# Kernel optimization log

Measured on AMD Instinct MI355X. Metric: run time of the kernel, lower is better.

## Reference

```python
import jax, jax.numpy as jnp
import numpy as np

B, S, D, H, DFF = 2, 2048, 2048, 16, 8192
DH = D // H
EPS = 1e-5


def _layer_norm(x, g, b):
    mu = jnp.mean(x, axis=-1, keepdims=True)
    var = jnp.mean(jnp.square(x - mu), axis=-1, keepdims=True)
    return (x - mu) * jax.lax.rsqrt(var + EPS) * g + b


def setup_inputs() -> dict:
    key = jax.random.key(0)
    ks = jax.random.split(key, 12)
    sc = 0.02
    inp = {
        "x": jax.random.normal(ks[0], (B, S, D), dtype=jnp.float32),
        # attention projections, stored [in, out] (torch Linear weight transposed)
        "wq": jax.random.normal(ks[1], (D, D), dtype=jnp.float32) * sc,
        "bq": jnp.zeros((D,), jnp.float32),
        "wk": jax.random.normal(ks[2], (D, D), dtype=jnp.float32) * sc,
        "bk": jnp.zeros((D,), jnp.float32),
        "wv": jax.random.normal(ks[3], (D, D), dtype=jnp.float32) * sc,
        "bv": jnp.zeros((D,), jnp.float32),
        "wo": jax.random.normal(ks[4], (D, D), dtype=jnp.float32) * sc,
        "bo": jnp.zeros((D,), jnp.float32),
        "ln1_g": jnp.ones((D,), jnp.float32),
        "ln1_b": jnp.zeros((D,), jnp.float32),
        # feed-forward
        "w1": jax.random.normal(ks[5], (D, DFF), dtype=jnp.float32) * sc,
        "b1": jnp.zeros((DFF,), jnp.float32),
        "w2": jax.random.normal(ks[6], (DFF, D), dtype=jnp.float32) * sc,
        "b2": jnp.zeros((D,), jnp.float32),
        "ln2_g": jnp.ones((D,), jnp.float32),
        "ln2_b": jnp.zeros((D,), jnp.float32),
    }
    return inp


def reference(x, wq, bq, wk, bk, wv, bv, wo, bo, ln1_g, ln1_b,
              w1, b1, w2, b2, ln2_g, ln2_b):
    # ---- MultiHeadAttentionBlock: x + MHA(LN(x)) ----
    h = _layer_norm(x, ln1_g, ln1_b)                      # [B,S,D]
    q = (h @ wq + bq).reshape(B, S, H, DH).transpose(0, 2, 1, 3)  # [B,H,S,DH]
    k = (h @ wk + bk).reshape(B, S, H, DH).transpose(0, 2, 1, 3)
    v = (h @ wv + bv).reshape(B, S, H, DH).transpose(0, 2, 1, 3)

    # faithful to source: scale by sqrt(d_dim), NOT sqrt(head_dim)
    scores = jnp.einsum("bhqd,bhkd->bhqk", q, k) / np.sqrt(D).astype(np.float32)
    # faithful triu/transpose masking (softmax sees raw zeros, not -inf)
    t = jnp.triu(scores).swapaxes(-2, -1)                 # [B,H,S,S]
    s = jax.nn.softmax(t, axis=-2)
    r = jnp.triu(s).swapaxes(-2, -1)
    attn = jnp.einsum("bhqk,bhkd->bhqd", r, v)            # [B,H,S,DH]
    attn = attn.transpose(0, 2, 1, 3).reshape(B, S, D)
    x = x + attn @ wo + bo

    # ---- FeedForwardBlock: x + FF(LN(x)), dropout rate 0 ----
    h2 = _layer_norm(x, ln2_g, ln2_b)
    ff = jax.nn.relu(h2 @ w1 + b1) @ w2 + b2
    return x + ff
```

## Files before the change

kernel.cpp:

```cpp
#include <hip/hip_runtime.h>


typedef unsigned short ushort_t;
typedef unsigned int   uint32;
typedef __attribute__((ext_vector_type(8))) short    short8;
typedef __attribute__((ext_vector_type(8))) ushort_t ushort8;
typedef __attribute__((ext_vector_type(4))) float    f32x4;

#define BDIM   2
#define SEQ    2048
#define DMODEL 2048
#define NHEAD  16
#define DHEAD  128
#define DFFN   8192
#define MROWS  (BDIM*SEQ)

#define GPTR(p) (const __attribute__((address_space(1))) void*)((const void*)(p))
#define SPTR(p) (__attribute__((address_space(3))) void*)((void*)(p))

__device__ __forceinline__ float bf2f(ushort_t u) {
  union { uint32 i; float f; } c; c.i = ((uint32)u) << 16; return c.f;
}
__device__ __forceinline__ ushort_t f2bf(float f) {
  union { float f; uint32 i; } c; c.f = f;
  uint32 u = c.i;
  return (ushort_t)((u + 0x7fffu + ((u >> 16) & 1u)) >> 16);
}

__global__ __launch_bounds__(256) void transpose_f32_bf16_kern(
    const float* __restrict__ W, ushort_t* __restrict__ Wt, int K, int N)
{
  __shared__ float tile[32][33];
  const int nb = blockIdx.x * 32, kb = blockIdx.y * 32;
  const int tx = threadIdx.x & 31, ty = threadIdx.x >> 5;
#pragma unroll
  for (int j = 0; j < 32; j += 8)
    tile[ty + j][tx] = W[(size_t)(kb + ty + j) * N + nb + tx];
  __syncthreads();
#pragma unroll
  for (int j = 0; j < 32; j += 8)
    Wt[(size_t)(nb + ty + j) * K + kb + tx] = f2bf(tile[tx][ty + j]);
}

__global__ __launch_bounds__(256) void ln_kern(
    const float* __restrict__ X, const float* __restrict__ G,
    const float* __restrict__ Bb, ushort_t* __restrict__ Out)
{
  const int row = blockIdx.x, tid = threadIdx.x;
  const float* xr = X + (size_t)row * DMODEL;
  float4 v0 = ((const float4*)xr)[tid * 2];
  float4 v1 = ((const float4*)xr)[tid * 2 + 1];
  float s  = v0.x + v0.y + v0.z + v0.w + v1.x + v1.y + v1.z + v1.w;
  float ss = v0.x*v0.x + v0.y*v0.y + v0.z*v0.z + v0.w*v0.w
           + v1.x*v1.x + v1.y*v1.y + v1.z*v1.z + v1.w*v1.w;
#pragma unroll
  for (int off = 32; off > 0; off >>= 1) {
    s  += __shfl_down(s, off);
    ss += __shfl_down(ss, off);
  }
  __shared__ float rs[4], rss[4];
  __shared__ float sh_mu, sh_rst;
  const int wv = tid >> 6;
  if ((tid & 63) == 0) { rs[wv] = s; rss[wv] = ss; }
  __syncthreads();
  if (tid == 0) {
    float S1 = rs[0] + rs[1] + rs[2] + rs[3];
    float S2 = rss[0] + rss[1] + rss[2] + rss[3];
    float mu = S1 * (1.f / DMODEL);
    float var = S2 * (1.f / DMODEL) - mu * mu;
    sh_mu = mu;
    sh_rst = rsqrtf(var + 1e-5f);
  }
  __syncthreads();
  const float mu = sh_mu, rst = sh_rst;
  float4 g0 = ((const float4*)G)[tid * 2];
  float4 g1 = ((const float4*)G)[tid * 2 + 1];
  float4 b0 = ((const float4*)Bb)[tid * 2];
  float4 b1 = ((const float4*)Bb)[tid * 2 + 1];
  ushort8 o;
  o[0] = f2bf((v0.x - mu) * rst * g0.x + b0.x);
  o[1] = f2bf((v0.y - mu) * rst * g0.y + b0.y);
  o[2] = f2bf((v0.z - mu) * rst * g0.z + b0.z);
  o[3] = f2bf((v0.w - mu) * rst * g0.w + b0.w);
  o[4] = f2bf((v1.x - mu) * rst * g1.x + b1.x);
  o[5] = f2bf((v1.y - mu) * rst * g1.y + b1.y);
  o[6] = f2bf((v1.z - mu) * rst * g1.z + b1.z);
  o[7] = f2bf((v1.w - mu) * rst * g1.w + b1.w);
  *(ushort8*)(Out + (size_t)row * DMODEL + tid * 8) = o;
}

template<int OUT_BF16, int RELU, int RESID>
__global__ __launch_bounds__(512, 2) void gemm_pipe_kern(
    const ushort_t* __restrict__ A, const ushort_t* __restrict__ Bt,
    const float* __restrict__ bias, const float* __restrict__ resid,
    void* __restrict__ Cout, int M, int N, int K)
{
  __shared__ ushort_t sA[3 * 128 * 32];
  __shared__ ushort_t sB[3 * 256 * 32];

  const int tid = threadIdx.x;
  const int nbx = gridDim.x;
  const int nwg = nbx * gridDim.y;
  const int bid = blockIdx.y * nbx + blockIdx.x;
  const int cpx = nwg >> 3;
  const int swz = (bid & 7) * cpx + (bid >> 3);
  const int n0 = (swz % nbx) * 256;
  const int m0 = (swz / nbx) * 128;

  const int l  = tid & 63, w = tid >> 6;
  const int lr = l & 15, lg = l >> 4;
  const int wr = w >> 2, wc = w & 3;

  const int srow = tid >> 2;
  const int schunk = ((tid & 3) ^ ((tid >> 3) & 3)) * 8;
  const ushort_t* Asrc  = A  + (size_t)(m0 + srow) * K + schunk;
  const ushort_t* Bsrc0 = Bt + (size_t)(n0 + srow) * K + schunk;
  const ushort_t* Bsrc1 = Bt + (size_t)(n0 + 128 + srow) * K + schunk;
  ushort_t* sAd = sA + tid * 8;
  ushort_t* sBd = sB + tid * 8;

  const int rdoff = ((lg ^ ((lr >> 1) & 3))) * 8;
  const int arow = (wr * 64 + lr) * 32 + rdoff;
  const int brow = (wc * 64 + lr) * 32 + rdoff;

  f32x4 acc[4][4] = {};
  const int T = K >> 5;

#define STAGE_AB0(d, kt) do { \
    __builtin_amdgcn_global_load_lds(GPTR(Asrc  + (size_t)(kt) * 32), SPTR(sAd + (d) * 4096), 16, 0, 0); \
    __builtin_amdgcn_global_load_lds(GPTR(Bsrc0 + (size_t)(kt) * 32), SPTR(sBd + (d) * 8192), 16, 0, 0); \
  } while (0)
#define STAGE_B1(d, kt) \
    __builtin_amdgcn_global_load_lds(GPTR(Bsrc1 + (size_t)(kt) * 32), SPTR(sBd + (d) * 8192 + 4096), 16, 0, 0)

  STAGE_AB0(0, 0); STAGE_B1(0, 0);
  STAGE_AB0(1, 1); STAGE_B1(1, 1);
  asm volatile("s_waitcnt vmcnt(3)" ::: "memory");
  __builtin_amdgcn_s_barrier();
  __builtin_amdgcn_sched_barrier(0);

  int cur = 0;
  for (int t = 0; t < T; ++t) {
    const int nxt2 = (cur == 0) ? 2 : cur - 1;
    const ushort_t* pA = sA + cur * 4096;
    const ushort_t* pB = sB + cur * 8192;

    short8 af0 = *(const short8*)(pA + arow);
    short8 af1 = *(const short8*)(pA + arow + 512);
    short8 af2 = *(const short8*)(pA + arow + 1024);
    short8 af3 = *(const short8*)(pA + arow + 1536);
    short8 bf0 = *(const short8*)(pB + brow);
    short8 bf1 = *(const short8*)(pB + brow + 512);
    if (t + 2 < T) STAGE_AB0(nxt2, t + 2);
    __builtin_amdgcn_s_barrier();
    asm volatile("s_waitcnt lgkmcnt(0)" ::: "memory");
    __builtin_amdgcn_sched_barrier(0);
    __builtin_amdgcn_s_setprio(1);
    acc[0][0] = __builtin_amdgcn_mfma_f32_16x16x32_bf16(af0, bf0, acc[0][0], 0, 0, 0);
    acc[1][0] = __builtin_amdgcn_mfma_f32_16x16x32_bf16(af1, bf0, acc[1][0], 0, 0, 0);
    acc[2][0] = __builtin_amdgcn_mfma_f32_16x16x32_bf16(af2, bf0, acc[2][0], 0, 0, 0);
    acc[3][0] = __builtin_amdgcn_mfma_f32_16x16x32_bf16(af3, bf0, acc[3][0], 0, 0, 0);
    acc[0][1] = __builtin_amdgcn_mfma_f32_16x16x32_bf16(af0, bf1, acc[0][1], 0, 0, 0);
    acc[1][1] = __builtin_amdgcn_mfma_f32_16x16x32_bf16(af1, bf1, acc[1][1], 0, 0, 0);
    acc[2][1] = __builtin_amdgcn_mfma_f32_16x16x32_bf16(af2, bf1, acc[2][1], 0, 0, 0);
    acc[3][1] = __builtin_amdgcn_mfma_f32_16x16x32_bf16(af3, bf1, acc[3][1], 0, 0, 0);
    __builtin_amdgcn_s_setprio(0);
    __builtin_amdgcn_s_barrier();

    short8 bf2 = *(const short8*)(pB + brow + 1024);
    short8 bf3 = *(const short8*)(pB + brow + 1536);
    if (t + 2 < T) STAGE_B1(nxt2, t + 2);
    __builtin_amdgcn_s_barrier();
    asm volatile("s_waitcnt lgkmcnt(0)" ::: "memory");
    __builtin_amdgcn_sched_barrier(0);
    __builtin_amdgcn_s_setprio(1);
    acc[0][2] = __builtin_amdgcn_mfma_f32_16x16x32_bf16(af0, bf2, acc[0][2], 0, 0, 0);
    acc[1][2] = __builtin_amdgcn_mfma_f32_16x16x32_bf16(af1, bf2, acc[1][2], 0, 0, 0);
    acc[2][2] = __builtin_amdgcn_mfma_f32_16x16x32_bf16(af2, bf2, acc[2][2], 0, 0, 0);
    acc[3][2] = __builtin_amdgcn_mfma_f32_16x16x32_bf16(af3, bf2, acc[3][2], 0, 0, 0);
    acc[0][3] = __builtin_amdgcn_mfma_f32_16x16x32_bf16(af0, bf3, acc[0][3], 0, 0, 0);
    acc[1][3] = __builtin_amdgcn_mfma_f32_16x16x32_bf16(af1, bf3, acc[1][3], 0, 0, 0);
    acc[2][3] = __builtin_amdgcn_mfma_f32_16x16x32_bf16(af2, bf3, acc[2][3], 0, 0, 0);
    acc[3][3] = __builtin_amdgcn_mfma_f32_16x16x32_bf16(af3, bf3, acc[3][3], 0, 0, 0);
    __builtin_amdgcn_s_setprio(0);
    if (t + 2 < T) { asm volatile("s_waitcnt vmcnt(3)" ::: "memory"); }
    else           { asm volatile("s_waitcnt vmcnt(0)" ::: "memory"); }
    __builtin_amdgcn_s_barrier();
    __builtin_amdgcn_sched_barrier(0);
    cur = (cur == 2) ? 0 : cur + 1;
  }
#undef STAGE_AB0
#undef STAGE_B1

#pragma unroll
  for (int mi = 0; mi < 4; ++mi) {
#pragma unroll
    for (int ni = 0; ni < 4; ++ni) {
      const int gn = n0 + wc * 64 + ni * 16 + lr;
      const float bvv = bias[gn];
#pragma unroll
      for (int j = 0; j < 4; ++j) {
        const int gm = m0 + wr * 64 + mi * 16 + lg * 4 + j;
        float v = acc[mi][ni][j] + bvv;
        if (RESID) v += resid[(size_t)gm * N + gn];
        if (RELU) v = fmaxf(v, 0.f);
        if (OUT_BF16) ((ushort_t*)Cout)[(size_t)gm * N + gn] = f2bf(v);
        else          ((float*)Cout)[(size_t)gm * N + gn] = v;
      }
    }
  }
}

__global__ __launch_bounds__(256) void attn_stats_kern(
    const ushort_t* __restrict__ Q, const ushort_t* __restrict__ Kb,
    float* __restrict__ E, float* __restrict__ DG)
{
  __shared__ ushort_t Ksm[64 * 128];
  const int qb = blockIdx.x;
  const int bh = blockIdx.y;
  const int b = bh >> 4, h = bh & 15;
  const int tid = threadIdx.x;
  const int l = tid & 63, w = tid >> 6;
  const int lr = l & 15, lg = l >> 4;

  const int qrow0 = qb * 64 + w * 16;

  const size_t qoff = (size_t)(b * SEQ + qrow0 + lr) * DMODEL + h * DHEAD + lg * 8;
  short8 af[4];
#pragma unroll
  for (int c = 0; c < 4; ++c) af[c] = *(const short8*)(Q + qoff + c * 32);

  const int srow_b = w * 16 + (l >> 4);
  const ushort_t* Kg = Kb + (size_t)b * SEQ * DMODEL + (size_t)h * DHEAD;
  ushort_t* Sbase = Ksm + w * 2048;

  f32x4 sume = {0.f, 0.f, 0.f, 0.f};
  f32x4 dge  = {0.f, 0.f, 0.f, 0.f};
  const float scale = 0.0220970869120796f;
  const int rx = lr & 7;

  for (int kc = qb; kc < 32; ++kc) {
    __syncthreads();
#pragma unroll
    for (int c = 0; c < 4; ++c) {
      const int row = srow_b + c * 4;
      const int g = (l & 15) ^ (row & 7);
      __builtin_amdgcn_global_load_lds(
          GPTR(Kg + (size_t)(kc * 64 + row) * DMODEL + g * 8),
          SPTR(Sbase + c * 512), 16, 0, 0);
    }
    __syncthreads();

    const int ks0 = (kc == qb) ? w : 0;
    for (int ks = ks0; ks < 4; ++ks) {
      short8 bfr[4];
#pragma unroll
      for (int c = 0; c < 4; ++c)
        bfr[c] = *(const short8*)(Ksm + (ks * 16 + lr) * 128 + ((lg + c * 4) ^ rx) * 8);
      f32x4 sc = {0.f, 0.f, 0.f, 0.f};
      sc = __builtin_amdgcn_mfma_f32_16x16x32_bf16(af[0], bfr[0], sc, 0, 0, 0);
      sc = __builtin_amdgcn_mfma_f32_16x16x32_bf16(af[1], bfr[1], sc, 0, 0, 0);
      sc = __builtin_amdgcn_mfma_f32_16x16x32_bf16(af[2], bfr[2], sc, 0, 0, 0);
      sc = __builtin_amdgcn_mfma_f32_16x16x32_bf16(af[3], bfr[3], sc, 0, 0, 0);
      if (kc == qb && ks == w) {
        const int ki = kc * 64 + ks * 16 + lr;
#pragma unroll
        for (int j = 0; j < 4; ++j) {
          const int qi = qrow0 + lg * 4 + j;
          if (ki >= qi) {
            float e = __expf(sc[j] * scale);
            sume[j] += e;
            if (ki == qi) dge[j] += e;
          }
        }
      } else {
#pragma unroll
        for (int j = 0; j < 4; ++j)
          sume[j] += __expf(sc[j] * scale);
      }
    }
  }

#pragma unroll
  for (int j = 0; j < 4; ++j) {
#pragma unroll
    for (int off = 1; off < 16; off <<= 1) {
      sume[j] += __shfl_xor(sume[j], off);
      dge[j]  += __shfl_xor(dge[j], off);
    }
  }
  if (lr == 0) {
#pragma unroll
    for (int j = 0; j < 4; ++j) {
      E[(size_t)bh * SEQ + qrow0 + lg * 4 + j]  = sume[j];
      DG[(size_t)bh * SEQ + qrow0 + lg * 4 + j] = dge[j];
    }
  }
}

__global__ __launch_bounds__(128) void vchunk_kern(
    const ushort_t* __restrict__ V, float* __restrict__ CS)
{
  const int c = blockIdx.x, bh = blockIdx.y;
  const int b = bh >> 4, h = bh & 15;
  const int dh = threadIdx.x;
  const ushort_t* vp = V + (size_t)(b * SEQ + c * 64) * DMODEL + h * DHEAD + dh;
  float s = 0.f;
  for (int i = 0; i < 64; ++i) s += bf2f(vp[(size_t)i * DMODEL]);
  CS[((size_t)bh * 32 + c) * 128 + dh] = s;
}

__global__ __launch_bounds__(128) void attn_combine_kern(
    const ushort_t* __restrict__ V, const float* __restrict__ CS,
    const float* __restrict__ E, const float* __restrict__ DG,
    ushort_t* __restrict__ Attn)
{
  const int c = blockIdx.x, bh = blockIdx.y;
  const int b = bh >> 4, h = bh & 15;
  const int dh = threadIdx.x;
  float prefix = 0.f;
  for (int cc = 0; cc < c; ++cc) prefix += CS[((size_t)bh * 32 + cc) * 128 + dh];
  const ushort_t* vp = V + (size_t)(b * SEQ + c * 64) * DMODEL + h * DHEAD + dh;
  ushort_t* ap = Attn + (size_t)(b * SEQ + c * 64) * DMODEL + h * DHEAD + dh;
  const int qb = c * 64;
  for (int i = 0; i < 64; ++i) {
    const int qq = qb + i;
    const float denom = (float)qq + E[(size_t)bh * SEQ + qq];
    const float de = DG[(size_t)bh * SEQ + qq];
    const float vv = bf2f(vp[(size_t)i * DMODEL]);
    ap[(size_t)i * DMODEL] = f2bf((prefix + de * vv) / denom);
    prefix += vv;
  }
}

extern "C" void kernel_launch(void* const* d_in, const int* in_sizes, int n_in,
                              void* d_out, int out_size, void* d_ws, size_t ws_size,
                              hipStream_t stream)
{
  const float* x    = (const float*)d_in[0];
  const float* wq   = (const float*)d_in[1];
  const float* bq   = (const float*)d_in[2];
  const float* wk   = (const float*)d_in[3];
  const float* bk   = (const float*)d_in[4];
  const float* wv   = (const float*)d_in[5];
  const float* bv   = (const float*)d_in[6];
  const float* wo   = (const float*)d_in[7];
  const float* bo   = (const float*)d_in[8];
  const float* ln1g = (const float*)d_in[9];
  const float* ln1b = (const float*)d_in[10];
  const float* w1   = (const float*)d_in[11];
  const float* b1   = (const float*)d_in[12];
  const float* w2   = (const float*)d_in[13];
  const float* b2   = (const float*)d_in[14];
  const float* ln2g = (const float*)d_in[15];
  const float* ln2b = (const float*)d_in[16];
  float* out = (float*)d_out;

  char* ws = (char*)d_ws;
  ushort_t* W1T  = (ushort_t*)(ws + 0);
  ushort_t* W2T  = (ushort_t*)(ws + 33554432);
  ushort_t* WOT  = (ushort_t*)(ws + 67108864);
  float*    X2   = (float*)   (ws + 75497472);
  ushort_t* Hb   = (ushort_t*)(ws + 109051904);
  ushort_t* F1   = (ushort_t*)(ws + 125829120);
  ushort_t* WQT  = (ushort_t*)(ws + 125829120);
  ushort_t* WKT  = (ushort_t*)(ws + 134217728);
  ushort_t* WVT  = (ushort_t*)(ws + 142606336);
  ushort_t* Qb   = (ushort_t*)(ws + 150994944);
  ushort_t* Kbuf = (ushort_t*)(ws + 167772160);
  ushort_t* Vb   = (ushort_t*)(ws + 184549376);
  float*    Eb   = (float*)   (ws + 201326592);
  float*    DGb  = (float*)   (ws + 201588736);
  float*    CSb  = (float*)   (ws + 201850880);

  transpose_f32_bf16_kern<<<dim3(64, 64),  256, 0, stream>>>(wq, WQT, 2048, 2048);
  transpose_f32_bf16_kern<<<dim3(64, 64),  256, 0, stream>>>(wk, WKT, 2048, 2048);
  transpose_f32_bf16_kern<<<dim3(64, 64),  256, 0, stream>>>(wv, WVT, 2048, 2048);
  transpose_f32_bf16_kern<<<dim3(64, 64),  256, 0, stream>>>(wo, WOT, 2048, 2048);
  transpose_f32_bf16_kern<<<dim3(256, 64), 256, 0, stream>>>(w1, W1T, 2048, 8192);
  transpose_f32_bf16_kern<<<dim3(64, 256), 256, 0, stream>>>(w2, W2T, 8192, 2048);

  ln_kern<<<MROWS, 256, 0, stream>>>(x, ln1g, ln1b, Hb);

  gemm_pipe_kern<1, 0, 0><<<dim3(8, 32), 512, 0, stream>>>(Hb, WQT, bq, nullptr, Qb,   MROWS, DMODEL, DMODEL);
  gemm_pipe_kern<1, 0, 0><<<dim3(8, 32), 512, 0, stream>>>(Hb, WKT, bk, nullptr, Kbuf, MROWS, DMODEL, DMODEL);
  gemm_pipe_kern<1, 0, 0><<<dim3(8, 32), 512, 0, stream>>>(Hb, WVT, bv, nullptr, Vb,   MROWS, DMODEL, DMODEL);

  attn_stats_kern<<<dim3(32, 32), 256, 0, stream>>>(Qb, Kbuf, Eb, DGb);

  vchunk_kern<<<dim3(32, 32), 128, 0, stream>>>(Vb, CSb);
  attn_combine_kern<<<dim3(32, 32), 128, 0, stream>>>(Vb, CSb, Eb, DGb, Hb);

  gemm_pipe_kern<0, 0, 1><<<dim3(8, 32), 512, 0, stream>>>(Hb, WOT, bo, x, X2, MROWS, DMODEL, DMODEL);

  ln_kern<<<MROWS, 256, 0, stream>>>(X2, ln2g, ln2b, Hb);

  gemm_pipe_kern<1, 1, 0><<<dim3(32, 32), 512, 0, stream>>>(Hb, W1T, b1, nullptr, F1, MROWS, DFFN, DMODEL);

  gemm_pipe_kern<0, 0, 1><<<dim3(8, 32), 512, 0, stream>>>(F1, W2T, b2, X2, out, MROWS, DMODEL, DFFN);
}
```

Baseline: 743.4 us.

## Fuse QKV projections into one GEMM and deepen GEMM K-tile to 64

Concatenates the Q, K and V weight matrices and their biases so a single GEMM with N=6144 produces all three projections into one interleaved buffer. The attention kernels take a leading-dimension parameter to read from it. The shared GEMM kernel now stages 64-wide K tiles with an 8-chunk XOR swizzle, uses a new column-major tile swizzle, and drops the min-blocks launch bound. The larger LDS footprint (about 144KB for the triple buffers) likely limits each CU to one workgroup, trading occupancy for fewer barriers per K step and fewer launches.

```diff
diff --git a/kernel.cpp b/kernel.cpp
--- a/kernel.cpp
+++ b/kernel.cpp
@@ -14,6 +14,7 @@
 #define DHEAD  128
 #define DFFN   8192
 #define MROWS  (BDIM*SEQ)
+#define LDQKV  6144
 
 #define GPTR(p) (const __attribute__((address_space(1))) void*)((const void*)(p))
 #define SPTR(p) (__attribute__((address_space(3))) void*)((void*)(p))
@@ -40,6 +41,14 @@
 #pragma unroll
   for (int j = 0; j < 32; j += 8)
     Wt[(size_t)(nb + ty + j) * K + kb + tx] = f2bf(tile[tx][ty + j]);
+}
+
+__global__ __launch_bounds__(256) void bias_concat_kern(
+    const float* __restrict__ a, const float* __restrict__ b,
+    const float* __restrict__ c, float* __restrict__ o)
+{
+  const int i = blockIdx.x * 256 + threadIdx.x;
+  o[i] = (i < 2048) ? a[i] : ((i < 4096) ? b[i - 2048] : c[i - 4096]);
 }
 
 __global__ __launch_bounds__(256) void ln_kern(
@@ -90,107 +99,134 @@
 }
 
 template<int OUT_BF16, int RELU, int RESID>
-__global__ __launch_bounds__(512, 2) void gemm_pipe_kern(
+__global__ __launch_bounds__(512) void gemm_pipe_kern(
     const ushort_t* __restrict__ A, const ushort_t* __restrict__ Bt,
     const float* __restrict__ bias, const float* __restrict__ resid,
     void* __restrict__ Cout, int M, int N, int K)
 {
-  __shared__ ushort_t sA[3 * 128 * 32];
-  __shared__ ushort_t sB[3 * 256 * 32];
+  __shared__ ushort_t sA[3 * 128 * 64];
+  __shared__ ushort_t sB[3 * 256 * 64];
 
   const int tid = threadIdx.x;
-  const int nbx = gridDim.x;
-  const int nwg = nbx * gridDim.y;
-  const int bid = blockIdx.y * nbx + blockIdx.x;
+  const int nM  = gridDim.y;
+  const int nwg = gridDim.x * nM;
+  const int bid = blockIdx.y * gridDim.x + blockIdx.x;
   const int cpx = nwg >> 3;
   const int swz = (bid & 7) * cpx + (bid >> 3);
-  const int n0 = (swz % nbx) * 256;
-  const int m0 = (swz / nbx) * 128;
+  const int m0 = (swz % nM) * 128;
+  const int n0 = (swz / nM) * 256;
 
   const int l  = tid & 63, w = tid >> 6;
   const int lr = l & 15, lg = l >> 4;
   const int wr = w >> 2, wc = w & 3;
 
-  const int srow = tid >> 2;
-  const int schunk = ((tid & 3) ^ ((tid >> 3) & 3)) * 8;
-  const ushort_t* Asrc  = A  + (size_t)(m0 + srow) * K + schunk;
-  const ushort_t* Bsrc0 = Bt + (size_t)(n0 + srow) * K + schunk;
-  const ushort_t* Bsrc1 = Bt + (size_t)(n0 + 128 + srow) * K + schunk;
+  const int srow  = tid >> 3;
+  const int schunk = (tid & 7) ^ (srow & 7);
+  const ushort_t* Asrc = A  + (size_t)(m0 + srow) * K + schunk * 8;
+  const ushort_t* Bsrc = Bt + (size_t)(n0 + srow) * K + schunk * 8;
   ushort_t* sAd = sA + tid * 8;
   ushort_t* sBd = sB + tid * 8;
 
-  const int rdoff = ((lg ^ ((lr >> 1) & 3))) * 8;
-  const int arow = (wr * 64 + lr) * 32 + rdoff;
-  const int brow = (wc * 64 + lr) * 32 + rdoff;
+  const int rxk  = lr & 7;
+  const int aoff = (wr * 64 + lr) * 64;
+  const int boff = (wc * 64 + lr) * 64;
 
   f32x4 acc[4][4] = {};
-  const int T = K >> 5;
-
-#define STAGE_AB0(d, kt) do { \
-    __builtin_amdgcn_global_load_lds(GPTR(Asrc  + (size_t)(kt) * 32), SPTR(sAd + (d) * 4096), 16, 0, 0); \
-    __builtin_amdgcn_global_load_lds(GPTR(Bsrc0 + (size_t)(kt) * 32), SPTR(sBd + (d) * 8192), 16, 0, 0); \
-  } while (0)
-#define STAGE_B1(d, kt) \
-    __builtin_amdgcn_global_load_lds(GPTR(Bsrc1 + (size_t)(kt) * 32), SPTR(sBd + (d) * 8192 + 4096), 16, 0, 0)
-
-  STAGE_AB0(0, 0); STAGE_B1(0, 0);
-  STAGE_AB0(1, 1); STAGE_B1(1, 1);
-  asm volatile("s_waitcnt vmcnt(3)" ::: "memory");
+  const int T = K >> 6;
+
+#define STAGE_A(d, kt, r) __builtin_amdgcn_global_load_lds( \
+    GPTR(Asrc + (size_t)(kt) * 64 + (size_t)(r) * 64 * K), \
+    SPTR(sAd + (d) * 8192 + (r) * 4096), 16, 0, 0)
+#define STAGE_B(d, kt, r) __builtin_amdgcn_global_load_lds( \
+    GPTR(Bsrc + (size_t)(kt) * 64 + (size_t)(r) * 64 * K), \
+    SPTR(sBd + (d) * 16384 + (r) * 4096), 16, 0, 0)
+
+  STAGE_A(0, 0, 0); STAGE_A(0, 0, 1);
+  STAGE_B(0, 0, 0); STAGE_B(0, 0, 1); STAGE_B(0, 0, 2); STAGE_B(0, 0, 3);
+  STAGE_A(1, 1, 0); STAGE_A(1, 1, 1);
+  STAGE_B(1, 1, 0); STAGE_B(1, 1, 1); STAGE_B(1, 1, 2); STAGE_B(1, 1, 3);
+  asm volatile("s_waitcnt vmcnt(6)" ::: "memory");
   __builtin_amdgcn_s_barrier();
   __builtin_amdgcn_sched_barrier(0);
 
   int cur = 0;
   for (int t = 0; t < T; ++t) {
-    const int nxt2 = (cur == 0) ? 2 : cur - 1;
-    const ushort_t* pA = sA + cur * 4096;
-    const ushort_t* pB = sB + cur * 8192;
-
-    short8 af0 = *(const short8*)(pA + arow);
-    short8 af1 = *(const short8*)(pA + arow + 512);
-    short8 af2 = *(const short8*)(pA + arow + 1024);
-    short8 af3 = *(const short8*)(pA + arow + 1536);
-    short8 bf0 = *(const short8*)(pB + brow);
-    short8 bf1 = *(const short8*)(pB + brow + 512);
-    if (t + 2 < T) STAGE_AB0(nxt2, t + 2);
+    const int nx = (cur == 0) ? 2 : cur - 1;
+    const ushort_t* pA = sA + cur * 8192;
+    const ushort_t* pB = sB + cur * 16384;
+    const bool pf = (t + 2 < T);
+
+    short8 a0 = *(const short8*)(pA + aoff +    0 + ((0 ^ rxk)) * 8 + (lg ^ 0) * 0);
+    a0 = *(const short8*)(pA + aoff +    0 + ((lg ^ rxk)) * 8);
+    short8 a1 = *(const short8*)(pA + aoff + 1024 + ((lg ^ rxk)) * 8);
+    short8 a2 = *(const short8*)(pA + aoff + 2048 + ((lg ^ rxk)) * 8);
+    short8 a3 = *(const short8*)(pA + aoff + 3072 + ((lg ^ rxk)) * 8);
+    short8 b0 = *(const short8*)(pB + boff +    0 + ((lg ^ rxk)) * 8);
+    short8 b1 = *(const short8*)(pB + boff + 1024 + ((lg ^ rxk)) * 8);
+    short8 b2 = *(const short8*)(pB + boff + 2048 + ((lg ^ rxk)) * 8);
+    short8 b3 = *(const short8*)(pB + boff + 3072 + ((lg ^ rxk)) * 8);
+    if (pf) { STAGE_A(nx, t + 2, 0); STAGE_A(nx, t + 2, 1); STAGE_B(nx, t + 2, 0); }
     __builtin_amdgcn_s_barrier();
     asm volatile("s_waitcnt lgkmcnt(0)" ::: "memory");
     __builtin_amdgcn_sched_barrier(0);
     __builtin_amdgcn_s_setprio(1);
-    acc[0][0] = __builtin_amdgcn_mfma_f32_16x16x32_bf16(af0, bf0, acc[0][0], 0, 0, 0);
-    acc[1][0] = __builtin_amdgcn_mfma_f32_16x16x32_bf16(af1, bf0, acc[1][0], 0, 0, 0);
-    acc[2][0] = __builtin_amdgcn_mfma_f32_16x16x32_bf16(af2, bf0, acc[2][0], 0, 0, 0);
-    acc[3][0] = __builtin_amdgcn_mfma_f32_16x16x32_bf16(af3, bf0, acc[3][0], 0, 0, 0);
-    acc[0][1] = __builtin_amdgcn_mfma_f32_16x16x32_bf16(af0, bf1, acc[0][1], 0, 0, 0);
-    acc[1][1] = __builtin_amdgcn_mfma_f32_16x16x32_bf16(af1, bf1, acc[1][1], 0, 0, 0);
-    acc[2][1] = __builtin_amdgcn_mfma_f32_16x16x32_bf16(af2, bf1, acc[2][1], 0, 0, 0);
-    acc[3][1] = __builtin_amdgcn_mfma_f32_16x16x32_bf16(af3, bf1, acc[3][1], 0, 0, 0);
+    acc[0][0] = __builtin_amdgcn_mfma_f32_16x16x32_bf16(a0, b0, acc[0][0], 0, 0, 0);
+    acc[1][0] = __builtin_amdgcn_mfma_f32_16x16x32_bf16(a1, b0, acc[1][0], 0, 0, 0);
+    acc[2][0] = __builtin_amdgcn_mfma_f32_16x16x32_bf16(a2, b0, acc[2][0], 0, 0, 0);
+    acc[3][0] = __builtin_amdgcn_mfma_f32_16x16x32_bf16(a3, b0, acc[3][0], 0, 0, 0);
+    acc[0][1] = __builtin_amdgcn_mfma_f32_16x16x32_bf16(a0, b1, acc[0][1], 0, 0, 0);
+    acc[1][1] = __builtin_amdgcn_mfma_f32_16x16x32_bf16(a1, b1, acc[1][1], 0, 0, 0);
+    acc[2][1] = __builtin_amdgcn_mfma_f32_16x16x32_bf16(a2, b1, acc[2][1], 0, 0, 0);
+    acc[3][1] = __builtin_amdgcn_mfma_f32_16x16x32_bf16(a3, b1, acc[3][1], 0, 0, 0);
+    acc[0][2] = __builtin_amdgcn_mfma_f32_16x16x32_bf16(a0, b2, acc[0][2], 0, 0, 0);
+    acc[1][2] = __builtin_amdgcn_mfma_f32_16x16x32_bf16(a1, b2, acc[1][2], 0, 0, 0);
+    acc[2][2] = __builtin_amdgcn_mfma_f32_16x16x32_bf16(a2, b2, acc[2][2], 0, 0, 0);
+    acc[3][2] = __builtin_amdgcn_mfma_f32_16x16x32_bf16(a3, b2, acc[3][2], 0, 0, 0);
+    acc[0][3] = __builtin_amdgcn_mfma_f32_16x16x32_bf16(a0, b3, acc[0][3], 0, 0, 0);
+    acc[1][3] = __builtin_amdgcn_mfma_f32_16x16x32_bf16(a1, b3, acc[1][3], 0, 0, 0);
+    acc[2][3] = __builtin_amdgcn_mfma_f32_16x16x32_bf16(a2, b3, acc[2][3], 0, 0, 0);
+    acc[3][3] = __builtin_amdgcn_mfma_f32_16x16x32_bf16(a3, b3, acc[3][3], 0, 0, 0);
     __builtin_amdgcn_s_setprio(0);
     __builtin_amdgcn_s_barrier();
 
-    short8 bf2 = *(const short8*)(pB + brow + 1024);
-    short8 bf3 = *(const short8*)(pB + brow + 1536);
-    if (t + 2 < T) STAGE_B1(nxt2, t + 2);
+    a0 = *(const short8*)(pA + aoff +    0 + (((4 + lg) ^ rxk)) * 8);
+    a1 = *(const short8*)(pA + aoff + 1024 + (((4 + lg) ^ rxk)) * 8);
+    a2 = *(const short8*)(pA + aoff + 2048 + (((4 + lg) ^ rxk)) * 8);
+    a3 = *(const short8*)(pA + aoff + 3072 + (((4 + lg) ^ rxk)) * 8);
+    b0 = *(const short8*)(pB + boff +    0 + (((4 + lg) ^ rxk)) * 8);
+    b1 = *(const short8*)(pB + boff + 1024 + (((4 + lg) ^ rxk)) * 8);
+    b2 = *(const short8*)(pB + boff + 2048 + (((4 + lg) ^ rxk)) * 8);
+    b3 = *(const short8*)(pB + boff + 3072 + (((4 + lg) ^ rxk)) * 8);
+    if (pf) { STAGE_B(nx, t + 2, 1); STAGE_B(nx, t + 2, 2); STAGE_B(nx, t + 2, 3); }
     __builtin_amdgcn_s_barrier();
     asm volatile("s_waitcnt lgkmcnt(0)" ::: "memory");
     __builtin_amdgcn_sched_barrier(0);
     __builtin_amdgcn_s_setprio(1);
-    acc[0][2] = __builtin_amdgcn_mfma_f32_16x16x32_bf16(af0, bf2, acc[0][2], 0, 0, 0);
-    acc[1][2] = __builtin_amdgcn_mfma_f32_16x16x32_bf16(af1, bf2, acc[1][2], 0, 0, 0);
-    acc[2][2] = __builtin_amdgcn_mfma_f32_16x16x32_bf16(af2, bf2, acc[2][2], 0, 0, 0);
-    acc[3][2] = __builtin_amdgcn_mfma_f32_16x16x32_bf16(af3, bf2, acc[3][2], 0, 0, 0);
-    acc[0][3] = __builtin_amdgcn_mfma_f32_16x16x32_bf16(af0, bf3, acc[0][3], 0, 0, 0);
-    acc[1][3] = __builtin_amdgcn_mfma_f32_16x16x32_bf16(af1, bf3, acc[1][3], 0, 0, 0);
-    acc[2][3] = __builtin_amdgcn_mfma_f32_16x16x32_bf16(af2, bf3, acc[2][3], 0, 0, 0);
-    acc[3][3] = __builtin_amdgcn_mfma_f32_16x16x32_bf16(af3, bf3, acc[3][3], 0, 0, 0);
+    acc[0][0] = __builtin_amdgcn_mfma_f32_16x16x32_bf16(a0, b0, acc[0][0], 0, 0, 0);
+    acc[1][0] = __builtin_amdgcn_mfma_f32_16x16x32_bf16(a1, b0, acc[1][0], 0, 0, 0);
+    acc[2][0] = __builtin_amdgcn_mfma_f32_16x16x32_bf16(a2, b0, acc[2][0], 0, 0, 0);
+    acc[3][0] = __builtin_amdgcn_mfma_f32_16x16x32_bf16(a3, b0, acc[3][0], 0, 0, 0);
+    acc[0][1] = __builtin_amdgcn_mfma_f32_16x16x32_bf16(a0, b1, acc[0][1], 0, 0, 0);
+    acc[1][1] = __builtin_amdgcn_mfma_f32_16x16x32_bf16(a1, b1, acc[1][1], 0, 0, 0);
+    acc[2][1] = __builtin_amdgcn_mfma_f32_16x16x32_bf16(a2, b1, acc[2][1], 0, 0, 0);
+    acc[3][1] = __builtin_amdgcn_mfma_f32_16x16x32_bf16(a3, b1, acc[3][1], 0, 0, 0);
+    acc[0][2] = __builtin_amdgcn_mfma_f32_16x16x32_bf16(a0, b2, acc[0][2], 0, 0, 0);
+    acc[1][2] = __builtin_amdgcn_mfma_f32_16x16x32_bf16(a1, b2, acc[1][2], 0, 0, 0);
+    acc[2][2] = __builtin_amdgcn_mfma_f32_16x16x32_bf16(a2, b2, acc[2][2], 0, 0, 0);
+    acc[3][2] = __builtin_amdgcn_mfma_f32_16x16x32_bf16(a3, b2, acc[3][2], 0, 0, 0);
+    acc[0][3] = __builtin_amdgcn_mfma_f32_16x16x32_bf16(a0, b3, acc[0][3], 0, 0, 0);
+    acc[1][3] = __builtin_amdgcn_mfma_f32_16x16x32_bf16(a1, b3, acc[1][3], 0, 0, 0);
+    acc[2][3] = __builtin_amdgcn_mfma_f32_16x16x32_bf16(a2, b3, acc[2][3], 0, 0, 0);
+    acc[3][3] = __builtin_amdgcn_mfma_f32_16x16x32_bf16(a3, b3, acc[3][3], 0, 0, 0);
     __builtin_amdgcn_s_setprio(0);
-    if (t + 2 < T) { asm volatile("s_waitcnt vmcnt(3)" ::: "memory"); }
-    else           { asm volatile("s_waitcnt vmcnt(0)" ::: "memory"); }
+    if (pf) { asm volatile("s_waitcnt vmcnt(6)" ::: "memory"); }
+    else    { asm volatile("s_waitcnt vmcnt(0)" ::: "memory"); }
     __builtin_amdgcn_s_barrier();
     __builtin_amdgcn_sched_barrier(0);
     cur = (cur == 2) ? 0 : cur + 1;
   }
-#undef STAGE_AB0
-#undef STAGE_B1
+#undef STAGE_A
+#undef STAGE_B
 
 #pragma unroll
   for (int mi = 0; mi < 4; ++mi) {
@@ -213,7 +249,7 @@
 
 __global__ __launch_bounds__(256) void attn_stats_kern(
     const ushort_t* __restrict__ Q, const ushort_t* __restrict__ Kb,
-    float* __restrict__ E, float* __restrict__ DG)
+    float* __restrict__ E, float* __restrict__ DG, int ld)
 {
   __shared__ ushort_t Ksm[64 * 128];
   const int qb = blockIdx.x;
@@ -225,13 +261,13 @@
 
   const int qrow0 = qb * 64 + w * 16;
 
-  const size_t qoff = (size_t)(b * SEQ + qrow0 + lr) * DMODEL + h * DHEAD + lg * 8;
+  const size_t qoff = (size_t)(b * SEQ + qrow0 + lr) * ld + h * DHEAD + lg * 8;
   short8 af[4];
 #pragma unroll
   for (int c = 0; c < 4; ++c) af[c] = *(const short8*)(Q + qoff + c * 32);
 
   const int srow_b = w * 16 + (l >> 4);
-  const ushort_t* Kg = Kb + (size_t)b * SEQ * DMODEL + (size_t)h * DHEAD;
+  const ushort_t* Kg = Kb + (size_t)b * SEQ * ld + (size_t)h * DHEAD;
   ushort_t* Sbase = Ksm + w * 2048;
 
   f32x4 sume = {0.f, 0.f, 0.f, 0.f};
@@ -246,7 +282,7 @@
       const int row = srow_b + c * 4;
       const int g = (l & 15) ^ (row & 7);
       __builtin_amdgcn_global_load_lds(
-          GPTR(Kg + (size_t)(kc * 64 + row) * DMODEL + g * 8),
+          GPTR(Kg + (size_t)(kc * 64 + row) * ld + g * 8),
           SPTR(Sbase + c * 512), 16, 0, 0);
     }
     __syncthreads();
@@ -299,35 +335,35 @@
 }
 
 __global__ __launch_bounds__(128) void vchunk_kern(
-    const ushort_t* __restrict__ V, float* __restrict__ CS)
+    const ushort_t* __restrict__ V, float* __restrict__ CS, int ld)
 {
   const int c = blockIdx.x, bh = blockIdx.y;
   const int b = bh >> 4, h = bh & 15;
   const int dh = threadIdx.x;
-  const ushort_t* vp = V + (size_t)(b * SEQ + c * 64) * DMODEL + h * DHEAD + dh;
+  const ushort_t* vp = V + (size_t)(b * SEQ + c * 64) * ld + h * DHEAD + dh;
   float s = 0.f;
-  for (int i = 0; i < 64; ++i) s += bf2f(vp[(size_t)i * DMODEL]);
+  for (int i = 0; i < 64; ++i) s += bf2f(vp[(size_t)i * ld]);
   CS[((size_t)bh * 32 + c) * 128 + dh] = s;
 }
 
 __global__ __launch_bounds__(128) void attn_combine_kern(
     const ushort_t* __restrict__ V, const float* __restrict__ CS,
     const float* __restrict__ E, const float* __restrict__ DG,
-    ushort_t* __restrict__ Attn)
+    ushort_t* __restrict__ Attn, int ldv)
 {
   const int c = blockIdx.x, bh = blockIdx.y;
   const int b = bh >> 4, h = bh & 15;
   const int dh = threadIdx.x;
   float prefix = 0.f;
   for (int cc = 0; cc < c; ++cc) prefix += CS[((size_t)bh * 32 + cc) * 128 + dh];
-  const ushort_t* vp = V + (size_t)(b * SEQ + c * 64) * DMODEL + h * DHEAD + dh;
+  const ushort_t* vp = V + (size_t)(b * SEQ + c * 64) * ldv + h * DHEAD + dh;
   ushort_t* ap = Attn + (size_t)(b * SEQ + c * 64) * DMODEL + h * DHEAD + dh;
   const int qb = c * 64;
   for (int i = 0; i < 64; ++i) {
     const int qq = qb + i;
     const float denom = (float)qq + E[(size_t)bh * SEQ + qq];
     const float de = DG[(size_t)bh * SEQ + qq];
-    const float vv = bf2f(vp[(size_t)i * DMODEL]);
+    const float vv = bf2f(vp[(size_t)i * ldv]);
     ap[(size_t)i * DMODEL] = f2bf((prefix + de * vv) / denom);
     prefix += vv;
   }
@@ -361,35 +397,31 @@
   ushort_t* W2T  = (ushort_t*)(ws + 33554432);
   ushort_t* WOT  = (ushort_t*)(ws + 67108864);
   float*    X2   = (float*)   (ws + 75497472);
+  float*    Bcat = (float*)   (ws + 75497472);
   ushort_t* Hb   = (ushort_t*)(ws + 109051904);
   ushort_t* F1   = (ushort_t*)(ws + 125829120);
-  ushort_t* WQT  = (ushort_t*)(ws + 125829120);
-  ushort_t* WKT  = (ushort_t*)(ws + 134217728);
-  ushort_t* WVT  = (ushort_t*)(ws + 142606336);
-  ushort_t* Qb   = (ushort_t*)(ws + 150994944);
-  ushort_t* Kbuf = (ushort_t*)(ws + 167772160);
-  ushort_t* Vb   = (ushort_t*)(ws + 184549376);
+  ushort_t* WQKV = (ushort_t*)(ws + 125829120);
+  ushort_t* QKVb = (ushort_t*)(ws + 150994944);
   float*    Eb   = (float*)   (ws + 201326592);
   float*    DGb  = (float*)   (ws + 201588736);
   float*    CSb  = (float*)   (ws + 201850880);
 
-  transpose_f32_bf16_kern<<<dim3(64, 64),  256, 0, stream>>>(wq, WQT, 2048, 2048);
-  transpose_f32_bf16_kern<<<dim3(64, 64),  256, 0, stream>>>(wk, WKT, 2048, 2048);
-  transpose_f32_bf16_kern<<<dim3(64, 64),  256, 0, stream>>>(wv, WVT, 2048, 2048);
+  transpose_f32_bf16_kern<<<dim3(64, 64),  256, 0, stream>>>(wq, WQKV,                 2048, 2048);
+  transpose_f32_bf16_kern<<<dim3(64, 64),  256, 0, stream>>>(wk, WQKV + 2048 * 2048,   2048, 2048);
+  transpose_f32_bf16_kern<<<dim3(64, 64),  256, 0, stream>>>(wv, WQKV + 2 * 2048 * 2048, 2048, 2048);
   transpose_f32_bf16_kern<<<dim3(64, 64),  256, 0, stream>>>(wo, WOT, 2048, 2048);
   transpose_f32_bf16_kern<<<dim3(256, 64), 256, 0, stream>>>(w1, W1T, 2048, 8192);
   transpose_f32_bf16_kern<<<dim3(64, 256), 256, 0, stream>>>(w2, W2T, 8192, 2048);
+  bias_concat_kern<<<24, 256, 0, stream>>>(bq, bk, bv, Bcat);
 
   ln_kern<<<MROWS, 256, 0, stream>>>(x, ln1g, ln1b, Hb);
 
-  gemm_pipe_kern<1, 0, 0><<<dim3(8, 32), 512, 0, stream>>>(Hb, WQT, bq, nullptr, Qb,   MROWS, DMODEL, DMODEL);
-  gemm_pipe_kern<1, 0, 0><<<dim3(8, 32), 512, 0, stream>>>(Hb, WKT, bk, nullptr, Kbuf, MROWS, DMODEL, DMODEL);
-  gemm_pipe_kern<1, 0, 0><<<dim3(8, 32), 512, 0, stream>>>(Hb, WVT, bv, nullptr, Vb,   MROWS, DMODEL, DMODEL);
-
-  attn_stats_kern<<<dim3(32, 32), 256, 0, stream>>>(Qb, Kbuf, Eb, DGb);
-
-  vchunk_kern<<<dim3(32, 32), 128, 0, stream>>>(Vb, CSb);
-  attn_combine_kern<<<dim3(32, 32), 128, 0, stream>>>(Vb, CSb, Eb, DGb, Hb);
+  gemm_pipe_kern<1, 0, 0><<<dim3(24, 32), 512, 0, stream>>>(Hb, WQKV, Bcat, nullptr, QKVb, MROWS, LDQKV, DMODEL);
+
+  attn_stats_kern<<<dim3(32, 32), 256, 0, stream>>>(QKVb, QKVb + 2048, Eb, DGb, LDQKV);
+
+  vchunk_kern<<<dim3(32, 32), 128, 0, stream>>>(QKVb + 4096, CSb, LDQKV);
+  attn_combine_kern<<<dim3(32, 32), 128, 0, stream>>>(QKVb + 4096, CSb, Eb, DGb, Hb, LDQKV);
 
   gemm_pipe_kern<0, 0, 1><<<dim3(8, 32), 512, 0, stream>>>(Hb, WOT, bo, x, X2, MROWS, DMODEL, DMODEL);
 
```

Result: faster. 719.6 us (-3.2%).
